# Optimization experiments

Hardware: AMD Instinct MI355X
Metric: run time of the kernel (lower is better)

## Reference

```python
import jax, jax.numpy as jnp
import numpy as np

EPS = 1e-6
NEG = -1e9
RES_RATIO = 1.0  # res_ratio init arg
MAKE_SYM = True


def _ln(x, g, b):
    m = jnp.mean(x, axis=-1, keepdims=True)
    v = jnp.mean((x - m) ** 2, axis=-1, keepdims=True)
    return (x - m) * jax.lax.rsqrt(v + EPS) * g + b


def _sim(q, k, W1q, W1k, b1, W2, b2):
    # NN(concat([q,k])) with first dense split into query/key halves:
    # relu(q@W1q + k@W1k + b1) @ W2 + b2  -> avoids materializing the 2d concat.
    qa = q @ W1q  # [b,n,sq,h]
    kb = k @ W1k  # [b,n,sk,h]
    h1 = jax.nn.relu(qa[:, :, :, None, :] + kb[:, :, None, :, :] + b1)  # [b,n,sq,sk,h]
    s = jnp.einsum('bnqkh,h->bnqk', h1, W2[:, 0]) + b2[0]
    if MAKE_SYM:
        qb = q @ W1k
        ka = k @ W1q
        h2 = jax.nn.relu(ka[:, :, None, :, :] + qb[:, :, :, None, :] + b1)
        s = s + jnp.einsum('bnqkh,h->bnqk', h2, W2[:, 0]) + b2[0]
    return s


def _attention(v, k, q, mask, Ww, bw, Wd, bd, W1q, W1k, b1, W2, b2):
    q = q @ Ww + bw
    k = k @ Ww + bw
    v = v @ Ww + bw
    logits = _sim(q, k, W1q, W1k, b1, W2, b2)
    if mask is not None:
        logits = logits + mask * NEG
    attn = jax.nn.softmax(logits, axis=-1)
    out = jnp.einsum('bnqk,bnkd->bnqd', attn, v)
    return out @ Wd + bd, attn


def setup_inputs() -> dict:
    key = jax.random.key(0)
    B, N, S, D, DFF, H = 4, 1, 256, 128, 512, 128
    ks = jax.random.split(key, 16)
    s = 0.02
    inp = {
        'x': jax.random.normal(ks[0], (B, N, S, D), jnp.float32),
        'enc_output': jax.random.normal(ks[1], (B, N, S, D), jnp.float32),
        'com_mask': jnp.zeros((B, N, S, S), jnp.float32),
        'dec_mask': jnp.zeros((B, N, S, S), jnp.float32),
        # shared pairwise-score MLP NN: Dense(H, relu) -> Dense(1)
        'W1q': jax.random.normal(ks[2], (D, H), jnp.float32) * s,
        'W1k': jax.random.normal(ks[3], (D, H), jnp.float32) * s,
        'b1': jnp.zeros((H,), jnp.float32),
        'W2': jax.random.normal(ks[4], (H, 1), jnp.float32) * s,
        'b2': jnp.zeros((1,), jnp.float32),
        # mha1 projections
        'Ww1': jax.random.normal(ks[5], (D, D), jnp.float32) * s,
        'bw1': jnp.zeros((D,), jnp.float32),
        'Wd1': jax.random.normal(ks[6], (D, D), jnp.float32) * s,
        'bd1': jnp.zeros((D,), jnp.float32),
        # mha2 projections
        'Ww2': jax.random.normal(ks[7], (D, D), jnp.float32) * s,
        'bw2': jnp.zeros((D,), jnp.float32),
        'Wd2': jax.random.normal(ks[8], (D, D), jnp.float32) * s,
        'bd2': jnp.zeros((D,), jnp.float32),
        # ffn
        'Wf1': jax.random.normal(ks[9], (D, DFF), jnp.float32) * s,
        'bf1': jnp.zeros((DFF,), jnp.float32),
        'Wf2': jax.random.normal(ks[10], (DFF, D), jnp.float32) * s,
        'bf2': jnp.zeros((D,), jnp.float32),
        # layernorms
        'ln1_g': jnp.ones((D,), jnp.float32), 'ln1_b': jnp.zeros((D,), jnp.float32),
        'ln2_g': jnp.ones((D,), jnp.float32), 'ln2_b': jnp.zeros((D,), jnp.float32),
        'ln3_g': jnp.ones((D,), jnp.float32), 'ln3_b': jnp.zeros((D,), jnp.float32),
    }
    return inp


def reference(x, enc_output, com_mask, dec_mask,
              W1q, W1k, b1, W2, b2,
              Ww1, bw1, Wd1, bd1,
              Ww2, bw2, Wd2, bd2,
              Wf1, bf1, Wf2, bf2,
              ln1_g, ln1_b, ln2_g, ln2_b, ln3_g, ln3_b):
    r = RES_RATIO
    # self-attention block (dropout inactive, eval mode)
    attn1, aw1 = _attention(x, x, x, com_mask, Ww1, bw1, Wd1, bd1, W1q, W1k, b1, W2, b2)
    out1 = _ln((2 - r) * attn1 + r * x, ln1_g, ln1_b)
    # cross-attention block
    attn2, aw2 = _attention(enc_output, enc_output, out1, dec_mask, Ww2, bw2, Wd2, bd2, W1q, W1k, b1, W2, b2)
    out2 = _ln((2 - r) * attn2 + r * out1, ln2_g, ln2_b)
    # ffn
    ffn = jax.nn.relu(out2 @ Wf1 + bf1) @ Wf2 + bf2
    out3 = _ln((2 - r) * ffn + r * out2, ln3_g, ln3_b)
    return out3
```

## Files before the change

### kernel.cpp

```cpp
#include <hip/hip_runtime.h>
#include <math.h>


#define LN_EPS 1e-6f
#define NEGV  (-1e9f)

constexpr int B = 4, S = 256, D = 128, H = 128, DFF = 512;
constexpr int R = B * S;

struct P {
    const float *x, *enc, *com_mask, *dec_mask;
    const float *W1q, *W1k, *b1, *W2;
    const float *Ww1, *bw1, *Wd1, *bd1;
    const float *Ww2, *bw2, *Wd2, *bd2;
    const float *Wf1, *bf1, *Wf2, *bf2;
    const float *ln1g, *ln1b, *ln2g, *ln2b, *ln3g, *ln3b;
    float *out;
    float *xw, *qa, *kb, *kv2w, *kb2, *ka2;
};

__global__ __launch_bounds__(512) void proj3_kernel(P p)
{
    const int g = blockIdx.y, tid = threadIdx.x;
    const int r0 = blockIdx.x * 8;
    __shared__ __align__(16) float Ash[8 * 128];
    __shared__ __align__(16) float Pw[8 * 128];
    __shared__ __align__(16) float Pp[2 * 8 * 128];

    const float* A    = g ? p.enc  : p.x;
    const float* Wp   = g ? p.Ww2  : p.Ww1;
    const float* bp   = g ? p.bw2  : p.bw1;
    float*       o_w  = g ? p.kv2w : p.xw;
    const float* Wsec = g ? p.W1k  : p.W1q;
    const float* bsec = g ? nullptr: p.b1;
    float*       o_s  = g ? p.kb2  : p.qa;
    const float* Wthr = g ? p.W1q  : p.W1k;
    float*       o_t  = g ? p.ka2  : p.kb;

    if (tid < 256)
        ((float4*)Ash)[tid] = ((const float4*)(A + (size_t)r0 * 128))[tid];
    __syncthreads();

    {
        const int kh = tid >> 8, unit = tid & 255, lr = unit >> 5, c4 = unit & 31;
        const float4* W4 = (const float4*)Wp;
        float4 acc = (kh == 0) ? ((const float4*)bp)[c4] : make_float4(0.f, 0.f, 0.f, 0.f);
        const int k0 = kh * 64;
        #pragma unroll 8
        for (int k = 0; k < 64; ++k) {
            const float a = Ash[lr * 128 + k0 + k];
            const float4 w = W4[(k0 + k) * 32 + c4];
            acc.x = fmaf(a, w.x, acc.x); acc.y = fmaf(a, w.y, acc.y);
            acc.z = fmaf(a, w.z, acc.z); acc.w = fmaf(a, w.w, acc.w);
        }
        ((float4*)Pp)[kh * 256 + unit] = acc;
    }
    __syncthreads();
    if (tid < 256) {
        const int lr = tid >> 5, c4 = tid & 31;
        const float4 a = ((const float4*)Pp)[tid];
        const float4 bq = ((const float4*)Pp)[256 + tid];
        const float4 w = make_float4(a.x + bq.x, a.y + bq.y, a.z + bq.z, a.w + bq.w);
        ((float4*)Pw)[tid] = w;
        ((float4*)o_w)[(size_t)(r0 + lr) * 32 + c4] = w;
    }
    __syncthreads();

    {
        const int which = tid >> 8, unit = tid & 255, lr = unit >> 5, c4 = unit & 31;
        const float* W = which ? Wthr : Wsec;
        const float* bb = which ? nullptr : bsec;
        float* o = which ? o_t : o_s;
        const float4* W4 = (const float4*)W;
        float4 acc = bb ? ((const float4*)bb)[c4] : make_float4(0.f, 0.f, 0.f, 0.f);
        #pragma unroll 8
        for (int k = 0; k < 128; ++k) {
            const float a = Pw[lr * 128 + k];
            const float4 w = W4[k * 32 + c4];
            acc.x = fmaf(a, w.x, acc.x); acc.y = fmaf(a, w.y, acc.y);
            acc.z = fmaf(a, w.z, acc.z); acc.w = fmaf(a, w.w, acc.w);
        }
        ((float4*)o)[(size_t)(r0 + lr) * 32 + c4] = acc;
    }
}

#define SC8(ACC, O1, X1, O2, X2)                                               \
    ACC = fmaf(fmaxf((O1).x + (X1).x, 0.f), w.x, ACC);                         \
    ACC = fmaf(fmaxf((O1).y + (X1).y, 0.f), w.y, ACC);                         \
    ACC = fmaf(fmaxf((O1).z + (X1).z, 0.f), w.z, ACC);                         \
    ACC = fmaf(fmaxf((O1).w + (X1).w, 0.f), w.w, ACC);                         \
    ACC = fmaf(fmaxf((O2).x + (X2).x, 0.f), w.x, ACC);                         \
    ACC = fmaf(fmaxf((O2).y + (X2).y, 0.f), w.y, ACC);                         \
    ACC = fmaf(fmaxf((O2).z + (X2).z, 0.f), w.z, ACC);                         \
    ACC = fmaf(fmaxf((O2).w + (X2).w, 0.f), w.w, ACC);

template<bool FIRST>
__device__ __forceinline__ void attn_stage(const P& p, float* smem,
                                           int tid, int r0, int bS)
{
    float* s8   = smem;
    float* rowS = smem + 1024;
    float* qa2L = smem + 18432;
    float* qb2L = smem + 18944;

    const float* __restrict__ S1g = FIRST ? p.kb : p.kb2;
    const float* __restrict__ S2g = FIRST ? p.qa : p.ka2;
    const float* mask = FIRST ? p.com_mask : p.dec_mask;
    const float* V    = FIRST ? p.xw : p.kv2w;
    const float* Wd   = FIRST ? p.Wd1 : p.Wd2;
    const float* bd   = FIRST ? p.bd1 : p.bd2;
    const float* lg   = FIRST ? p.ln1g : p.ln2g;
    const float* lb   = FIRST ? p.ln1b : p.ln2b;

    {
        const int hh = tid & 7, unit = tid >> 3, kk = unit & 31, rg = unit >> 5;
        const int rA = r0 + 2 * rg, rB = rA + 1;

        float4 o1A[4], o1B[4], o2A[4], o2B[4], w2r[4];
        #pragma unroll
        for (int j = 0; j < 4; ++j) {
            const int h = hh * 4 + 32 * j;
            if (FIRST) {
                o1A[j] = *(const float4*)(p.qa + (size_t)rA * H + h);
                o1B[j] = *(const float4*)(p.qa + (size_t)rB * H + h);
                o2A[j] = *(const float4*)(p.kb + (size_t)rA * H + h);
                o2B[j] = *(const float4*)(p.kb + (size_t)rB * H + h);
            } else {
                o1A[j] = *(const float4*)(qa2L + (2 * rg)     * H + h);
                o1B[j] = *(const float4*)(qa2L + (2 * rg + 1) * H + h);
                o2A[j] = *(const float4*)(qb2L + (2 * rg)     * H + h);
                o2B[j] = *(const float4*)(qb2L + (2 * rg + 1) * H + h);
            }
            w2r[j] = *(const float4*)(p.W2 + h);
        }

        for (int kt = 0; kt < 4; ++kt) {
            const float* __restrict__ r1a = S1g + (size_t)(bS + kt * 64 + kk)      * H;
            const float* __restrict__ r1b = S1g + (size_t)(bS + kt * 64 + kk + 32) * H;
            const float* __restrict__ r2a = S2g + (size_t)(bS + kt * 64 + kk)      * H;
            const float* __restrict__ r2b = S2g + (size_t)(bS + kt * 64 + kk + 32) * H;

            float4 x1a[4], x1b[4], x2a[4], x2b[4];
            #pragma unroll
            for (int j = 0; j < 4; ++j) {
                const int h = hh * 4 + 32 * j;
                x1a[j] = *(const float4*)(r1a + h);
                x1b[j] = *(const float4*)(r1b + h);
                x2a[j] = *(const float4*)(r2a + h);
                x2b[j] = *(const float4*)(r2b + h);
            }

            float aAa = 0.f, aAb = 0.f, aBa = 0.f, aBb = 0.f;
            #pragma unroll
            for (int j = 0; j < 4; ++j) {
                const float4 w = w2r[j];
                SC8(aAa, o1A[j], x1a[j], o2A[j], x2a[j])
                SC8(aAb, o1A[j], x1b[j], o2A[j], x2b[j])
                SC8(aBa, o1B[j], x1a[j], o2B[j], x2a[j])
                SC8(aBb, o1B[j], x1b[j], o2B[j], x2b[j])
            }
            #pragma unroll
            for (int o = 1; o < 8; o <<= 1) {
                aAa += __shfl_xor(aAa, o, 8);
                aAb += __shfl_xor(aAb, o, 8);
                aBa += __shfl_xor(aBa, o, 8);
                aBb += __shfl_xor(aBb, o, 8);
            }
            if (hh == 0) {
                const int kb0 = kt * 64;
                s8[(2 * rg)     * 256 + kb0 + kk]      = aAa;
                s8[(2 * rg)     * 256 + kb0 + kk + 32] = aAb;
                s8[(2 * rg + 1) * 256 + kb0 + kk]      = aBa;
                s8[(2 * rg + 1) * 256 + kb0 + kk + 32] = aBb;
            }
        }
    }
    __syncthreads();

    for (int i = tid; i < 1024; i += 512) {
        const int r = i >> 8, k = i & 255;
        s8[i] += mask[(size_t)(r0 + r) * S + k] * NEGV;
    }
    __syncthreads();

    {
        const int g = tid >> 6, c = tid & 63;
        if (g < 4) {
            float* rowp = s8 + g * 256;
            float m = -INFINITY;
            #pragma unroll
            for (int k = c; k < 256; k += 64) m = fmaxf(m, rowp[k]);
            for (int o = 32; o; o >>= 1) m = fmaxf(m, __shfl_xor(m, o, 64));
            float s = 0.f;
            #pragma unroll
            for (int k = c; k < 256; k += 64) { const float e = __expf(rowp[k] - m); rowp[k] = e; s += e; }
            for (int o = 32; o; o >>= 1) s += __shfl_xor(s, o, 64);
            const float rinv = 1.f / s;
            #pragma unroll
            for (int k = c; k < 256; k += 64) rowp[k] *= rinv;
        }
    }
    __syncthreads();

    float* avp = smem + 1536;
    float* aoS = smem + 3584;
    float* pp  = smem + 4096;

    {
        const int r = tid >> 7, t = tid & 127, kq = t >> 5, c4 = t & 31;
        const float4* V4 = (const float4*)(V + (size_t)bS * D);
        const float* sp = s8 + r * 256 + kq * 64;
        float4 acc = make_float4(0.f, 0.f, 0.f, 0.f);
        #pragma unroll 8
        for (int k = 0; k < 64; ++k) {
            const float a = sp[k];
            const float4 v = V4[(kq * 64 + k) * 32 + c4];
            acc.x = fmaf(a, v.x, acc.x); acc.y = fmaf(a, v.y, acc.y);
            acc.z = fmaf(a, v.z, acc.z); acc.w = fmaf(a, v.w, acc.w);
        }
        ((float4*)avp)[(r * 4 + kq) * 32 + c4] = acc;
    }
    __syncthreads();
    if (tid < 128) {
        const int r = tid >> 5, c4 = tid & 31;
        float4 s0 = ((const float4*)avp)[(r * 4 + 0) * 32 + c4];
        const float4 s1 = ((const float4*)avp)[(r * 4 + 1) * 32 + c4];
        const float4 s2 = ((const float4*)avp)[(r * 4 + 2) * 32 + c4];
        const float4 s3 = ((const float4*)avp)[(r * 4 + 3) * 32 + c4];
        s0.x += s1.x + s2.x + s3.x; s0.y += s1.y + s2.y + s3.y;
        s0.z += s1.z + s2.z + s3.z; s0.w += s1.w + s2.w + s3.w;
        ((float4*)aoS)[r * 32 + c4] = s0;
    }
    __syncthreads();

    {
        const int kq = tid >> 7, unit = tid & 127, r = unit >> 5, c4 = unit & 31;
        const float4* W4 = (const float4*)Wd;
        const float* ap = aoS + r * 128 + kq * 32;
        float4 acc = make_float4(0.f, 0.f, 0.f, 0.f);
        #pragma unroll 8
        for (int k = 0; k < 32; ++k) {
            const float a = ap[k];
            const float4 w = W4[(kq * 32 + k) * 32 + c4];
            acc.x = fmaf(a, w.x, acc.x); acc.y = fmaf(a, w.y, acc.y);
            acc.z = fmaf(a, w.z, acc.z); acc.w = fmaf(a, w.w, acc.w);
        }
        ((float4*)pp)[kq * 128 + unit] = acc;
    }
    __syncthreads();

    if (tid < 128) {
        const int r = tid >> 5, c4 = tid & 31;
        const float4 p0 = ((const float4*)pp)[tid];
        const float4 p1 = ((const float4*)pp)[128 + tid];
        const float4 p2 = ((const float4*)pp)[256 + tid];
        const float4 p3 = ((const float4*)pp)[384 + tid];
        const float4 bv0 = ((const float4*)bd)[c4];
        float4 r4;
        if (FIRST) r4 = ((const float4*)(p.x + (size_t)(r0 + r) * 128))[c4];
        else       r4 = ((const float4*)rowS)[r * 32 + c4];
        const float x0 = p0.x + p1.x + p2.x + p3.x + bv0.x + r4.x;
        const float x1 = p0.y + p1.y + p2.y + p3.y + bv0.y + r4.y;
        const float x2 = p0.z + p1.z + p2.z + p3.z + bv0.z + r4.z;
        const float x3 = p0.w + p1.w + p2.w + p3.w + bv0.w + r4.w;
        float s  = x0 + x1 + x2 + x3;
        float s2 = x0 * x0 + x1 * x1 + x2 * x2 + x3 * x3;
        for (int o = 16; o; o >>= 1) { s += __shfl_xor(s, o, 32); s2 += __shfl_xor(s2, o, 32); }
        const float m = s * (1.f / 128), var = s2 * (1.f / 128) - m * m;
        const float rs = rsqrtf(var + LN_EPS);
        const float4 gv = ((const float4*)lg)[c4], bv = ((const float4*)lb)[c4];
        float4 o4;
        o4.x = (x0 - m) * rs * gv.x + bv.x; o4.y = (x1 - m) * rs * gv.y + bv.y;
        o4.z = (x2 - m) * rs * gv.z + bv.z; o4.w = (x3 - m) * rs * gv.w + bv.w;
        ((float4*)rowS)[r * 32 + c4] = o4;
    }
    __syncthreads();

    if (FIRST) {
        float* qpp  = smem + 6144;
        float* q2wS = smem + 8192;
        float* qp2  = smem + 8704;
        {
            const int kq = tid >> 7, unit = tid & 127, r = unit >> 5, c4 = unit & 31;
            const float4* W4 = (const float4*)p.Ww2;
            const float* ap = rowS + r * 128 + kq * 32;
            float4 acc = make_float4(0.f, 0.f, 0.f, 0.f);
            #pragma unroll 8
            for (int k = 0; k < 32; ++k) {
                const float a = ap[k];
                const float4 w = W4[(kq * 32 + k) * 32 + c4];
                acc.x = fmaf(a, w.x, acc.x); acc.y = fmaf(a, w.y, acc.y);
                acc.z = fmaf(a, w.z, acc.z); acc.w = fmaf(a, w.w, acc.w);
            }
            ((float4*)qpp)[kq * 128 + unit] = acc;
        }
        __syncthreads();
        if (tid < 128) {
            const int c4 = tid & 31;
            const float4 p0 = ((const float4*)qpp)[tid];
            const float4 p1 = ((const float4*)qpp)[128 + tid];
            const float4 p2 = ((const float4*)qpp)[256 + tid];
            const float4 p3 = ((const float4*)qpp)[384 + tid];
            const float4 bw = ((const float4*)p.bw2)[c4];
            ((float4*)q2wS)[tid] = make_float4(p0.x + p1.x + p2.x + p3.x + bw.x,
                                               p0.y + p1.y + p2.y + p3.y + bw.y,
                                               p0.z + p1.z + p2.z + p3.z + bw.z,
                                               p0.w + p1.w + p2.w + p3.w + bw.w);
        }
        __syncthreads();
        {
            const int which = tid >> 8, sub = tid & 255;
            const int kh = sub >> 7, unit2 = sub & 127;
            const float4* W4 = (const float4*)(which ? p.W1k : p.W1q);
            const int r = unit2 >> 5;
            const float* ap = q2wS + r * 128 + kh * 64;
            float4 acc = make_float4(0.f, 0.f, 0.f, 0.f);
            #pragma unroll 8
            for (int k = 0; k < 64; ++k) {
                const float a = ap[k];
                const float4 w = W4[(kh * 64 + k) * 32 + (unit2 & 31)];
                acc.x = fmaf(a, w.x, acc.x); acc.y = fmaf(a, w.y, acc.y);
                acc.z = fmaf(a, w.z, acc.z); acc.w = fmaf(a, w.w, acc.w);
            }
            ((float4*)qp2)[(which * 2 + kh) * 128 + unit2] = acc;
        }
        __syncthreads();
        if (tid < 256) {
            const int which = tid >> 7, unit2 = tid & 127;
            const int c4 = unit2 & 31;
            const float4 p0 = ((const float4*)qp2)[(which * 2 + 0) * 128 + unit2];
            const float4 p1 = ((const float4*)qp2)[(which * 2 + 1) * 128 + unit2];
            const float4 b1v = ((const float4*)p.b1)[c4];
            float* oq = which ? qb2L : qa2L;
            ((float4*)oq)[unit2] =
                make_float4(p0.x + p1.x + b1v.x, p0.y + p1.y + b1v.y,
                            p0.z + p1.z + b1v.z, p0.w + p1.w + b1v.w);
        }
        __syncthreads();
    } else {
        float* hidP = smem + 1536;
        float* part = smem + 9984;
        {
            const int c = tid & 127, kh = tid >> 7;
            const float4* Wf1_4 = (const float4*)p.Wf1;
            float4 a0 = make_float4(0.f,0.f,0.f,0.f), a1 = a0, a2 = a0, a3 = a0;
            const int kbase = kh * 32;
            #pragma unroll 8
            for (int k = 0; k < 32; ++k) {
                const int kk = kbase + k;
                const float4 w = Wf1_4[kk * 128 + c];
                const float s0 = rowS[kk],       s1 = rowS[128 + kk];
                const float s2 = rowS[256 + kk], s3 = rowS[384 + kk];
                a0.x=fmaf(s0,w.x,a0.x); a0.y=fmaf(s0,w.y,a0.y); a0.z=fmaf(s0,w.z,a0.z); a0.w=fmaf(s0,w.w,a0.w);
                a1.x=fmaf(s1,w.x,a1.x); a1.y=fmaf(s1,w.y,a1.y); a1.z=fmaf(s1,w.z,a1.z); a1.w=fmaf(s1,w.w,a1.w);
                a2.x=fmaf(s2,w.x,a2.x); a2.y=fmaf(s2,w.y,a2.y); a2.z=fmaf(s2,w.z,a2.z); a2.w=fmaf(s2,w.w,a2.w);
                a3.x=fmaf(s3,w.x,a3.x); a3.y=fmaf(s3,w.y,a3.y); a3.z=fmaf(s3,w.z,a3.z); a3.w=fmaf(s3,w.w,a3.w);
            }
            float4* h4 = (float4*)hidP;
            const int base = kh * 512;
            h4[base + 0*128 + c] = a0; h4[base + 1*128 + c] = a1;
            h4[base + 2*128 + c] = a2; h4[base + 3*128 + c] = a3;
        }
        __syncthreads();
        for (int i = tid; i < 2048; i += 512) {
            hidP[i] = fmaxf(hidP[i] + hidP[2048 + i] + hidP[4096 + i] + hidP[6144 + i]
                            + p.bf1[i & 511], 0.f);
        }
        __syncthreads();
        {
            const int c4f = tid & 31, kg = tid >> 5;
            const float4* Wf2_4 = (const float4*)p.Wf2;
            float4 a0 = make_float4(0.f,0.f,0.f,0.f), a1 = a0, a2 = a0, a3 = a0;
            const int kbase = kg * 32;
            const float* h0 = hidP + 0 * 512 + kbase;
            const float* h1 = hidP + 1 * 512 + kbase;
            const float* h2 = hidP + 2 * 512 + kbase;
            const float* h3 = hidP + 3 * 512 + kbase;
            #pragma unroll 8
            for (int k = 0; k < 32; ++k) {
                const float4 w = Wf2_4[(kbase + k) * 32 + c4f];
                const float s0 = h0[k], s1 = h1[k], s2 = h2[k], s3 = h3[k];
                a0.x=fmaf(s0,w.x,a0.x); a0.y=fmaf(s0,w.y,a0.y); a0.z=fmaf(s0,w.z,a0.z); a0.w=fmaf(s0,w.w,a0.w);
                a1.x=fmaf(s1,w.x,a1.x); a1.y=fmaf(s1,w.y,a1.y); a1.z=fmaf(s1,w.z,a1.z); a1.w=fmaf(s1,w.w,a1.w);
                a2.x=fmaf(s2,w.x,a2.x); a2.y=fmaf(s2,w.y,a2.y); a2.z=fmaf(s2,w.z,a2.z); a2.w=fmaf(s2,w.w,a2.w);
                a3.x=fmaf(s3,w.x,a3.x); a3.y=fmaf(s3,w.y,a3.y); a3.z=fmaf(s3,w.z,a3.z); a3.w=fmaf(s3,w.w,a3.w);
            }
            float4* p4 = (float4*)part;
            p4[kg * 128 + 0 * 32 + c4f] = a0; p4[kg * 128 + 1 * 32 + c4f] = a1;
            p4[kg * 128 + 2 * 32 + c4f] = a2; p4[kg * 128 + 3 * 32 + c4f] = a3;
        }
        __syncthreads();
        if (tid < 128) {
            const int r = tid >> 5, c4 = tid & 31;
            const float4* p4 = (const float4*)part;
            float4 sum = ((const float4*)p.bf2)[c4];
            #pragma unroll
            for (int kg = 0; kg < 16; ++kg) {
                const float4 v = p4[kg * 128 + r * 32 + c4];
                sum.x += v.x; sum.y += v.y; sum.z += v.z; sum.w += v.w;
            }
            const float4 r4 = ((const float4*)rowS)[r * 32 + c4];
            const float x0 = sum.x + r4.x, x1 = sum.y + r4.y;
            const float x2 = sum.z + r4.z, x3 = sum.w + r4.w;
            float s  = x0 + x1 + x2 + x3;
            float s2 = x0 * x0 + x1 * x1 + x2 * x2 + x3 * x3;
            for (int o = 16; o; o >>= 1) { s += __shfl_xor(s, o, 32); s2 += __shfl_xor(s2, o, 32); }
            const float m = s * (1.f / 128), var = s2 * (1.f / 128) - m * m;
            const float rs = rsqrtf(var + LN_EPS);
            const float4 gv = ((const float4*)p.ln3g)[c4], bv = ((const float4*)p.ln3b)[c4];
            float4 o4;
            o4.x = (x0 - m) * rs * gv.x + bv.x; o4.y = (x1 - m) * rs * gv.y + bv.y;
            o4.z = (x2 - m) * rs * gv.z + bv.z; o4.w = (x3 - m) * rs * gv.w + bv.w;
            ((float4*)p.out)[(size_t)(r0 + r) * 32 + c4] = o4;
        }
    }
}

__global__ __launch_bounds__(512) void fused_attn12_kernel(P p)
{
    __shared__ __align__(16) float smem[19456];
    const int tid = threadIdx.x;
    const int r0 = blockIdx.x * 4, bS = (r0 >> 8) * S;
    attn_stage<true >(p, smem, tid, r0, bS);
    attn_stage<false>(p, smem, tid, r0, bS);
}

extern "C" void kernel_launch(void* const* d_in, const int* in_sizes, int n_in,
                              void* d_out, int out_size, void* d_ws, size_t ws_size,
                              hipStream_t stream) {
    (void)in_sizes; (void)n_in; (void)out_size; (void)ws_size;
    P p;
    p.x        = (const float*)d_in[0];
    p.enc      = (const float*)d_in[1];
    p.com_mask = (const float*)d_in[2];
    p.dec_mask = (const float*)d_in[3];
    p.W1q = (const float*)d_in[4];
    p.W1k = (const float*)d_in[5];
    p.b1  = (const float*)d_in[6];
    p.W2  = (const float*)d_in[7];
    p.Ww1 = (const float*)d_in[9];
    p.bw1 = (const float*)d_in[10];
    p.Wd1 = (const float*)d_in[11];
    p.bd1 = (const float*)d_in[12];
    p.Ww2 = (const float*)d_in[13];
    p.bw2 = (const float*)d_in[14];
    p.Wd2 = (const float*)d_in[15];
    p.bd2 = (const float*)d_in[16];
    p.Wf1 = (const float*)d_in[17];
    p.bf1 = (const float*)d_in[18];
    p.Wf2 = (const float*)d_in[19];
    p.bf2 = (const float*)d_in[20];
    p.ln1g = (const float*)d_in[21];
    p.ln1b = (const float*)d_in[22];
    p.ln2g = (const float*)d_in[23];
    p.ln2b = (const float*)d_in[24];
    p.ln3g = (const float*)d_in[25];
    p.ln3b = (const float*)d_in[26];
    p.out  = (float*)d_out;

    float* ws = (float*)d_ws;
    const size_t RD = (size_t)R * D;
    p.xw    = ws;
    p.qa    = p.xw    + RD;
    p.kb    = p.qa    + RD;
    p.kv2w  = p.kb    + RD;
    p.kb2   = p.kv2w  + RD;
    p.ka2   = p.kb2   + RD;

    proj3_kernel<<<dim3(R / 8, 2), 512, 0, stream>>>(p);
    fused_attn12_kernel<<<R / 4, 512, 0, stream>>>(p);
}
```

Measured before the change: 164.5 us.

## Halve rows per block in projection and fused attention kernels to double grid size

Both kernels now handle half as many rows per block (4 in the projection kernel, 2 in the attention kernel), so twice as many blocks are launched. Thread work is re-split into more K-slices with wider shared-memory partial reductions. The mask add is folded into the score write, softmax normalisation is deferred to a per-row reciprocal applied after attn·V, and the shared-memory footprint is shrunk. The aim is more blocks and better occupancy across the CUs, at the cost of reloading K/V and weights from global memory more often per row.

Measured after the change: 178.1 us. +8.2%, slower.

```diff
diff --git a/kernel.cpp b/kernel.cpp
--- a/kernel.cpp
+++ b/kernel.cpp
@@ -22,10 +22,11 @@
 __global__ __launch_bounds__(512) void proj3_kernel(P p)
 {
     const int g = blockIdx.y, tid = threadIdx.x;
-    const int r0 = blockIdx.x * 8;
-    __shared__ __align__(16) float Ash[8 * 128];
-    __shared__ __align__(16) float Pw[8 * 128];
-    __shared__ __align__(16) float Pp[2 * 8 * 128];
+    const int r0 = blockIdx.x * 4;
+    __shared__ __align__(16) float Ash[4 * 128];
+    __shared__ __align__(16) float Pw[4 * 128];
+    __shared__ __align__(16) float Pp[4 * 4 * 128];
+    __shared__ __align__(16) float P2[2 * 2 * 4 * 128];
 
     const float* A    = g ? p.enc  : p.x;
     const float* Wp   = g ? p.Ww2  : p.Ww1;
@@ -37,50 +38,67 @@
     const float* Wthr = g ? p.W1q  : p.W1k;
     float*       o_t  = g ? p.ka2  : p.kb;
 
-    if (tid < 256)
+    if (tid < 128)
         ((float4*)Ash)[tid] = ((const float4*)(A + (size_t)r0 * 128))[tid];
     __syncthreads();
 
     {
-        const int kh = tid >> 8, unit = tid & 255, lr = unit >> 5, c4 = unit & 31;
+        const int kh = tid >> 7, unit = tid & 127, lr = unit >> 5, c4 = unit & 31;
         const float4* W4 = (const float4*)Wp;
         float4 acc = (kh == 0) ? ((const float4*)bp)[c4] : make_float4(0.f, 0.f, 0.f, 0.f);
-        const int k0 = kh * 64;
+        const int k0 = kh * 32;
         #pragma unroll 8
-        for (int k = 0; k < 64; ++k) {
+        for (int k = 0; k < 32; ++k) {
             const float a = Ash[lr * 128 + k0 + k];
             const float4 w = W4[(k0 + k) * 32 + c4];
             acc.x = fmaf(a, w.x, acc.x); acc.y = fmaf(a, w.y, acc.y);
             acc.z = fmaf(a, w.z, acc.z); acc.w = fmaf(a, w.w, acc.w);
         }
-        ((float4*)Pp)[kh * 256 + unit] = acc;
-    }
-    __syncthreads();
-    if (tid < 256) {
+        ((float4*)Pp)[kh * 128 + unit] = acc;
+    }
+    __syncthreads();
+    if (tid < 128) {
         const int lr = tid >> 5, c4 = tid & 31;
-        const float4 a = ((const float4*)Pp)[tid];
-        const float4 bq = ((const float4*)Pp)[256 + tid];
-        const float4 w = make_float4(a.x + bq.x, a.y + bq.y, a.z + bq.z, a.w + bq.w);
+        const float4 a0 = ((const float4*)Pp)[tid];
+        const float4 a1 = ((const float4*)Pp)[128 + tid];
+        const float4 a2 = ((const float4*)Pp)[256 + tid];
+        const float4 a3 = ((const float4*)Pp)[384 + tid];
+        const float4 w = make_float4(a0.x + a1.x + a2.x + a3.x,
+                                     a0.y + a1.y + a2.y + a3.y,
+                                     a0.z + a1.z + a2.z + a3.z,
+                                     a0.w + a1.w + a2.w + a3.w);
         ((float4*)Pw)[tid] = w;
         ((float4*)o_w)[(size_t)(r0 + lr) * 32 + c4] = w;
     }
     __syncthreads();
 
     {
-        const int which = tid >> 8, unit = tid & 255, lr = unit >> 5, c4 = unit & 31;
+        const int which = tid >> 8, sub = tid & 255;
+        const int kh = sub >> 7, unit2 = sub & 127, lr = unit2 >> 5, c4 = unit2 & 31;
         const float* W = which ? Wthr : Wsec;
         const float* bb = which ? nullptr : bsec;
-        float* o = which ? o_t : o_s;
         const float4* W4 = (const float4*)W;
-        float4 acc = bb ? ((const float4*)bb)[c4] : make_float4(0.f, 0.f, 0.f, 0.f);
+        float4 acc = (kh == 0 && bb) ? ((const float4*)bb)[c4]
+                                     : make_float4(0.f, 0.f, 0.f, 0.f);
+        const int k0 = kh * 64;
         #pragma unroll 8
-        for (int k = 0; k < 128; ++k) {
-            const float a = Pw[lr * 128 + k];
-            const float4 w = W4[k * 32 + c4];
+        for (int k = 0; k < 64; ++k) {
+            const float a = Pw[lr * 128 + k0 + k];
+            const float4 w = W4[(k0 + k) * 32 + c4];
             acc.x = fmaf(a, w.x, acc.x); acc.y = fmaf(a, w.y, acc.y);
             acc.z = fmaf(a, w.z, acc.z); acc.w = fmaf(a, w.w, acc.w);
         }
-        ((float4*)o)[(size_t)(r0 + lr) * 32 + c4] = acc;
+        ((float4*)P2)[(which * 2 + kh) * 128 + unit2] = acc;
+    }
+    __syncthreads();
+    if (tid < 256) {
+        const int which = tid >> 7, unit2 = tid & 127;
+        const int lr = unit2 >> 5, c4 = unit2 & 31;
+        const float4 p0 = ((const float4*)P2)[(which * 2 + 0) * 128 + unit2];
+        const float4 p1 = ((const float4*)P2)[(which * 2 + 1) * 128 + unit2];
+        float* o = which ? o_t : o_s;
+        ((float4*)o)[(size_t)(r0 + lr) * 32 + c4] =
+            make_float4(p0.x + p1.x, p0.y + p1.y, p0.z + p1.z, p0.w + p1.w);
     }
 }
 
@@ -98,10 +116,12 @@
 __device__ __forceinline__ void attn_stage(const P& p, float* smem,
                                            int tid, int r0, int bS)
 {
-    float* s8   = smem;
-    float* rowS = smem + 1024;
-    float* qa2L = smem + 18432;
-    float* qb2L = smem + 18944;
+    float* s8    = smem;
+    float* rowS  = smem + 512;
+    float* rinvS = smem + 768;
+    float* qa2L  = smem + 784;
+    float* qb2L  = smem + 1040;
+    constexpr int SB = 1296;
 
     const float* __restrict__ S1g = FIRST ? p.kb : p.kb2;
     const float* __restrict__ S2g = FIRST ? p.qa : p.ka2;
@@ -113,8 +133,8 @@
     const float* lb   = FIRST ? p.ln1b : p.ln2b;
 
     {
-        const int hh = tid & 7, unit = tid >> 3, kk = unit & 31, rg = unit >> 5;
-        const int rA = r0 + 2 * rg, rB = rA + 1;
+        const int hh = tid & 7, kk = tid >> 3;
+        const int rA = r0, rB = r0 + 1;
 
         float4 o1A[4], o1B[4], o2A[4], o2B[4], w2r[4];
         #pragma unroll
@@ -126,66 +146,51 @@
                 o2A[j] = *(const float4*)(p.kb + (size_t)rA * H + h);
                 o2B[j] = *(const float4*)(p.kb + (size_t)rB * H + h);
             } else {
-                o1A[j] = *(const float4*)(qa2L + (2 * rg)     * H + h);
-                o1B[j] = *(const float4*)(qa2L + (2 * rg + 1) * H + h);
-                o2A[j] = *(const float4*)(qb2L + (2 * rg)     * H + h);
-                o2B[j] = *(const float4*)(qb2L + (2 * rg + 1) * H + h);
+                o1A[j] = *(const float4*)(qa2L + h);
+                o1B[j] = *(const float4*)(qa2L + 128 + h);
+                o2A[j] = *(const float4*)(qb2L + h);
+                o2B[j] = *(const float4*)(qb2L + 128 + h);
             }
             w2r[j] = *(const float4*)(p.W2 + h);
         }
 
+        #pragma unroll
         for (int kt = 0; kt < 4; ++kt) {
-            const float* __restrict__ r1a = S1g + (size_t)(bS + kt * 64 + kk)      * H;
-            const float* __restrict__ r1b = S1g + (size_t)(bS + kt * 64 + kk + 32) * H;
-            const float* __restrict__ r2a = S2g + (size_t)(bS + kt * 64 + kk)      * H;
-            const float* __restrict__ r2b = S2g + (size_t)(bS + kt * 64 + kk + 32) * H;
-
-            float4 x1a[4], x1b[4], x2a[4], x2b[4];
+            const float* __restrict__ r1 = S1g + (size_t)(bS + kt * 64 + kk) * H;
+            const float* __restrict__ r2 = S2g + (size_t)(bS + kt * 64 + kk) * H;
+
+            float4 x1[4], x2[4];
             #pragma unroll
             for (int j = 0; j < 4; ++j) {
                 const int h = hh * 4 + 32 * j;
-                x1a[j] = *(const float4*)(r1a + h);
-                x1b[j] = *(const float4*)(r1b + h);
-                x2a[j] = *(const float4*)(r2a + h);
-                x2b[j] = *(const float4*)(r2b + h);
-            }
-
-            float aAa = 0.f, aAb = 0.f, aBa = 0.f, aBb = 0.f;
+                x1[j] = *(const float4*)(r1 + h);
+                x2[j] = *(const float4*)(r2 + h);
+            }
+
+            float aA = 0.f, aB = 0.f;
             #pragma unroll
             for (int j = 0; j < 4; ++j) {
                 const float4 w = w2r[j];
-                SC8(aAa, o1A[j], x1a[j], o2A[j], x2a[j])
-                SC8(aAb, o1A[j], x1b[j], o2A[j], x2b[j])
-                SC8(aBa, o1B[j], x1a[j], o2B[j], x2a[j])
-                SC8(aBb, o1B[j], x1b[j], o2B[j], x2b[j])
+                SC8(aA, o1A[j], x1[j], o2A[j], x2[j])
+                SC8(aB, o1B[j], x1[j], o2B[j], x2[j])
             }
             #pragma unroll
             for (int o = 1; o < 8; o <<= 1) {
-                aAa += __shfl_xor(aAa, o, 8);
-                aAb += __shfl_xor(aAb, o, 8);
-                aBa += __shfl_xor(aBa, o, 8);
-                aBb += __shfl_xor(aBb, o, 8);
+                aA += __shfl_xor(aA, o, 8);
+                aB += __shfl_xor(aB, o, 8);
             }
             if (hh == 0) {
-                const int kb0 = kt * 64;
-                s8[(2 * rg)     * 256 + kb0 + kk]      = aAa;
-                s8[(2 * rg)     * 256 + kb0 + kk + 32] = aAb;
-                s8[(2 * rg + 1) * 256 + kb0 + kk]      = aBa;
-                s8[(2 * rg + 1) * 256 + kb0 + kk + 32] = aBb;
-            }
-        }
-    }
-    __syncthreads();
-
-    for (int i = tid; i < 1024; i += 512) {
-        const int r = i >> 8, k = i & 255;
-        s8[i] += mask[(size_t)(r0 + r) * S + k] * NEGV;
+                const int k = kt * 64 + kk;
+                s8[k]       = aA + mask[(size_t)rA * S + k] * NEGV;
+                s8[256 + k] = aB + mask[(size_t)rB * S + k] * NEGV;
+            }
+        }
     }
     __syncthreads();
 
     {
         const int g = tid >> 6, c = tid & 63;
-        if (g < 4) {
+        if (g < 2) {
             float* rowp = s8 + g * 256;
             float m = -INFINITY;
             #pragma unroll
@@ -195,74 +200,72 @@
             #pragma unroll
             for (int k = c; k < 256; k += 64) { const float e = __expf(rowp[k] - m); rowp[k] = e; s += e; }
             for (int o = 32; o; o >>= 1) s += __shfl_xor(s, o, 64);
-            const float rinv = 1.f / s;
-            #pragma unroll
-            for (int k = c; k < 256; k += 64) rowp[k] *= rinv;
-        }
-    }
-    __syncthreads();
-
-    float* avp = smem + 1536;
-    float* aoS = smem + 3584;
-    float* pp  = smem + 4096;
-
-    {
-        const int r = tid >> 7, t = tid & 127, kq = t >> 5, c4 = t & 31;
+            if (c == 0) rinvS[g] = 1.f / s;
+        }
+    }
+    __syncthreads();
+
+    float* avp = smem + SB;
+    float* aoS = smem + SB + 2048;
+    float* pp  = smem + SB + 2304;
+
+    {
+        const int r = tid >> 8, t = tid & 255, kq = t >> 5, c4 = t & 31;
         const float4* V4 = (const float4*)(V + (size_t)bS * D);
-        const float* sp = s8 + r * 256 + kq * 64;
-        float4 acc = make_float4(0.f, 0.f, 0.f, 0.f);
-        #pragma unroll 8
-        for (int k = 0; k < 64; ++k) {
-            const float a = sp[k];
-            const float4 v = V4[(kq * 64 + k) * 32 + c4];
-            acc.x = fmaf(a, v.x, acc.x); acc.y = fmaf(a, v.y, acc.y);
-            acc.z = fmaf(a, v.z, acc.z); acc.w = fmaf(a, v.w, acc.w);
-        }
-        ((float4*)avp)[(r * 4 + kq) * 32 + c4] = acc;
-    }
-    __syncthreads();
-    if (tid < 128) {
-        const int r = tid >> 5, c4 = tid & 31;
-        float4 s0 = ((const float4*)avp)[(r * 4 + 0) * 32 + c4];
-        const float4 s1 = ((const float4*)avp)[(r * 4 + 1) * 32 + c4];
-        const float4 s2 = ((const float4*)avp)[(r * 4 + 2) * 32 + c4];
-        const float4 s3 = ((const float4*)avp)[(r * 4 + 3) * 32 + c4];
-        s0.x += s1.x + s2.x + s3.x; s0.y += s1.y + s2.y + s3.y;
-        s0.z += s1.z + s2.z + s3.z; s0.w += s1.w + s2.w + s3.w;
-        ((float4*)aoS)[r * 32 + c4] = s0;
-    }
-    __syncthreads();
-
-    {
-        const int kq = tid >> 7, unit = tid & 127, r = unit >> 5, c4 = unit & 31;
-        const float4* W4 = (const float4*)Wd;
-        const float* ap = aoS + r * 128 + kq * 32;
+        const float* sp = s8 + r * 256 + kq * 32;
         float4 acc = make_float4(0.f, 0.f, 0.f, 0.f);
         #pragma unroll 8
         for (int k = 0; k < 32; ++k) {
+            const float a = sp[k];
+            const float4 v = V4[(kq * 32 + k) * 32 + c4];
+            acc.x = fmaf(a, v.x, acc.x); acc.y = fmaf(a, v.y, acc.y);
+            acc.z = fmaf(a, v.z, acc.z); acc.w = fmaf(a, v.w, acc.w);
+        }
+        ((float4*)avp)[(r * 8 + kq) * 32 + c4] = acc;
+    }
+    __syncthreads();
+    if (tid < 64) {
+        const int r = tid >> 5, c4 = tid & 31;
+        float4 s0 = make_float4(0.f, 0.f, 0.f, 0.f);
+        #pragma unroll
+        for (int i = 0; i < 8; ++i) {
+            const float4 v = ((const float4*)avp)[(r * 8 + i) * 32 + c4];
+            s0.x += v.x; s0.y += v.y; s0.z += v.z; s0.w += v.w;
+        }
+        const float rv = rinvS[r];
+        ((float4*)aoS)[r * 32 + c4] = make_float4(s0.x * rv, s0.y * rv, s0.z * rv, s0.w * rv);
+    }
+    __syncthreads();
+
+    {
+        const int kq = tid >> 6, unit = tid & 63, r = unit >> 5, c4 = unit & 31;
+        const float4* W4 = (const float4*)Wd;
+        const float* ap = aoS + r * 128 + kq * 16;
+        float4 acc = make_float4(0.f, 0.f, 0.f, 0.f);
+        #pragma unroll 8
+        for (int k = 0; k < 16; ++k) {
             const float a = ap[k];
-            const float4 w = W4[(kq * 32 + k) * 32 + c4];
+            const float4 w = W4[(kq * 16 + k) * 32 + c4];
             acc.x = fmaf(a, w.x, acc.x); acc.y = fmaf(a, w.y, acc.y);
             acc.z = fmaf(a, w.z, acc.z); acc.w = fmaf(a, w.w, acc.w);
         }
-        ((float4*)pp)[kq * 128 + unit] = acc;
-    }
-    __syncthreads();
-
-    if (tid < 128) {
+        ((float4*)pp)[kq * 64 + unit] = acc;
+    }
+    __syncthreads();
+
+    if (tid < 64) {
         const int r = tid >> 5, c4 = tid & 31;
-        const float4 p0 = ((const float4*)pp)[tid];
-        const float4 p1 = ((const float4*)pp)[128 + tid];
-        const float4 p2 = ((const float4*)pp)[256 + tid];
-        const float4 p3 = ((const float4*)pp)[384 + tid];
-        const float4 bv0 = ((const float4*)bd)[c4];
+        float4 sum = ((const float4*)bd)[c4];
+        #pragma unroll
+        for (int i = 0; i < 8; ++i) {
+            const float4 v = ((const float4*)pp)[i * 64 + tid];
+            sum.x += v.x; sum.y += v.y; sum.z += v.z; sum.w += v.w;
+        }
         float4 r4;
         if (FIRST) r4 = ((const float4*)(p.x + (size_t)(r0 + r) * 128))[c4];
         else       r4 = ((const float4*)rowS)[r * 32 + c4];
-        const float x0 = p0.x + p1.x + p2.x + p3.x + bv0.x + r4.x;
-        const float x1 = p0.y + p1.y + p2.y + p3.y + bv0.y + r4.y;
-        const float x2 = p0.z + p1.z + p2.z + p3.z + bv0.z + r4.z;
-        const float x3 = p0.w + p1.w + p2.w + p3.w + bv0.w + r4.w;
+        const float x0 = sum.x + r4.x, x1 = sum.y + r4.y;
+        const float x2 = sum.z + r4.z, x3 = sum.w + r4.w;
         float s  = x0 + x1 + x2 + x3;
         float s2 = x0 * x0 + x1 * x1 + x2 * x2 + x3 * x3;
         for (int o = 16; o; o >>= 1) { s += __shfl_xor(s, o, 32); s2 += __shfl_xor(s2, o, 32); }
@@ -277,126 +280,114 @@
     __syncthreads();
 
     if (FIRST) {
-        float* qpp  = smem + 6144;
-        float* q2wS = smem + 8192;
-        float* qp2  = smem + 8704;
+        float* qpp  = smem + SB;
+        float* q2wS = smem + SB + 2048;
+        float* qp2  = smem + SB + 2304;
         {
-            const int kq = tid >> 7, unit = tid & 127, r = unit >> 5, c4 = unit & 31;
+            const int kq = tid >> 6, unit = tid & 63, r = unit >> 5, c4 = unit & 31;
             const float4* W4 = (const float4*)p.Ww2;
-            const float* ap = rowS + r * 128 + kq * 32;
+            const float* ap = rowS + r * 128 + kq * 16;
+            float4 acc = make_float4(0.f, 0.f, 0.f, 0.f);
+            #pragma unroll 8
+            for (int k = 0; k < 16; ++k) {
+                const float a = ap[k];
+                const float4 w = W4[(kq * 16 + k) * 32 + c4];
+                acc.x = fmaf(a, w.x, acc.x); acc.y = fmaf(a, w.y, acc.y);
+                acc.z = fmaf(a, w.z, acc.z); acc.w = fmaf(a, w.w, acc.w);
+            }
+            ((float4*)qpp)[kq * 64 + unit] = acc;
+        }
+        __syncthreads();
+        if (tid < 64) {
+            const int c4 = tid & 31;
+            float4 sum = ((const float4*)p.bw2)[c4];
+            #pragma unroll
+            for (int i = 0; i < 8; ++i) {
+                const float4 v = ((const float4*)qpp)[i * 64 + tid];
+                sum.x += v.x; sum.y += v.y; sum.z += v.z; sum.w += v.w;
+            }
+            ((float4*)q2wS)[tid] = sum;
+        }
+        __syncthreads();
+        {
+            const int which = tid >> 8, sub = tid & 255;
+            const int kh = sub >> 6, unit2 = sub & 63, r = unit2 >> 5, c4 = unit2 & 31;
+            const float4* W4 = (const float4*)(which ? p.W1k : p.W1q);
+            const float* ap = q2wS + r * 128 + kh * 32;
             float4 acc = make_float4(0.f, 0.f, 0.f, 0.f);
             #pragma unroll 8
             for (int k = 0; k < 32; ++k) {
                 const float a = ap[k];
-                const float4 w = W4[(kq * 32 + k) * 32 + c4];
+                const float4 w = W4[(kh * 32 + k) * 32 + c4];
                 acc.x = fmaf(a, w.x, acc.x); acc.y = fmaf(a, w.y, acc.y);
                 acc.z = fmaf(a, w.z, acc.z); acc.w = fmaf(a, w.w, acc.w);
             }
-            ((float4*)qpp)[kq * 128 + unit] = acc;
+            ((float4*)qp2)[(which * 4 + kh) * 64 + unit2] = acc;
         }
         __syncthreads();
         if (tid < 128) {
-            const int c4 = tid & 31;
-            const float4 p0 = ((const float4*)qpp)[tid];
-            const float4 p1 = ((const float4*)qpp)[128 + tid];
-            const float4 p2 = ((const float4*)qpp)[256 + tid];
-            const float4 p3 = ((const float4*)qpp)[384 + tid];
-            const float4 bw = ((const float4*)p.bw2)[c4];
-            ((float4*)q2wS)[tid] = make_float4(p0.x + p1.x + p2.x + p3.x + bw.x,
-                                               p0.y + p1.y + p2.y + p3.y + bw.y,
-                                               p0.z + p1.z + p2.z + p3.z + bw.z,
-                                               p0.w + p1.w + p2.w + p3.w + bw.w);
-        }
-        __syncthreads();
-        {
-            const int which = tid >> 8, sub = tid & 255;
-            const int kh = sub >> 7, unit2 = sub & 127;
-            const float4* W4 = (const float4*)(which ? p.W1k : p.W1q);
-            const int r = unit2 >> 5;
-            const float* ap = q2wS + r * 128 + kh * 64;
-            float4 acc = make_float4(0.f, 0.f, 0.f, 0.f);
-            #pragma unroll 8
-            for (int k = 0; k < 64; ++k) {
-                const float a = ap[k];
-                const float4 w = W4[(kh * 64 + k) * 32 + (unit2 & 31)];
-                acc.x = fmaf(a, w.x, acc.x); acc.y = fmaf(a, w.y, acc.y);
-                acc.z = fmaf(a, w.z, acc.z); acc.w = fmaf(a, w.w, acc.w);
-            }
-            ((float4*)qp2)[(which * 2 + kh) * 128 + unit2] = acc;
-        }
-        __syncthreads();
-        if (tid < 256) {
-            const int which = tid >> 7, unit2 = tid & 127;
-            const int c4 = unit2 & 31;
-            const float4 p0 = ((const float4*)qp2)[(which * 2 + 0) * 128 + unit2];
-            const float4 p1 = ((const float4*)qp2)[(which * 2 + 1) * 128 + unit2];
-            const float4 b1v = ((const float4*)p.b1)[c4];
+            const int which = tid >> 6, unit2 = tid & 63, c4 = unit2 & 31;
+            float4 sum = ((const float4*)p.b1)[c4];
+            #pragma unroll
+            for (int i = 0; i < 4; ++i) {
+                const float4 v = ((const float4*)qp2)[(which * 4 + i) * 64 + unit2];
+                sum.x += v.x; sum.y += v.y; sum.z += v.z; sum.w += v.w;
+            }
             float* oq = which ? qb2L : qa2L;
-            ((float4*)oq)[unit2] =
-                make_float4(p0.x + p1.x + b1v.x, p0.y + p1.y + b1v.y,
-                            p0.z + p1.z + b1v.z, p0.w + p1.w + b1v.w);
+            ((float4*)oq)[unit2] = sum;
         }
         __syncthreads();
     } else {
-        float* hidP = smem + 1536;
-        float* part = smem + 9984;
+        float* hidP = smem + SB;
+        float* part = smem + SB + 4096;
         {
             const int c = tid & 127, kh = tid >> 7;
             const float4* Wf1_4 = (const float4*)p.Wf1;
-            float4 a0 = make_float4(0.f,0.f,0.f,0.f), a1 = a0, a2 = a0, a3 = a0;
+            float4 a0 = make_float4(0.f,0.f,0.f,0.f), a1 = a0;
             const int kbase = kh * 32;
             #pragma unroll 8
             for (int k = 0; k < 32; ++k) {
                 const int kk = kbase + k;
                 const float4 w = Wf1_4[kk * 128 + c];
-                const float s0 = rowS[kk],       s1 = rowS[128 + kk];
-                const float s2 = rowS[256 + kk], s3 = rowS[384 + kk];
+                const float s0 = rowS[kk], s1 = rowS[128 + kk];
                 a0.x=fmaf(s0,w.x,a0.x); a0.y=fmaf(s0,w.y,a0.y); a0.z=fmaf(s0,w.z,a0.z); a0.w=fmaf(s0,w.w,a0.w);
                 a1.x=fmaf(s1,w.x,a1.x); a1.y=fmaf(s1,w.y,a1.y); a1.z=fmaf(s1,w.z,a1.z); a1.w=fmaf(s1,w.w,a1.w);
-                a2.x=fmaf(s2,w.x,a2.x); a2.y=fmaf(s2,w.y,a2.y); a2.z=fmaf(s2,w.z,a2.z); a2.w=fmaf(s2,w.w,a2.w);
-                a3.x=fmaf(s3,w.x,a3.x); a3.y=fmaf(s3,w.y,a3.y); a3.z=fmaf(s3,w.z,a3.z); a3.w=fmaf(s3,w.w,a3.w);
             }
             float4* h4 = (float4*)hidP;
-            const int base = kh * 512;
-            h4[base + 0*128 + c] = a0; h4[base + 1*128 + c] = a1;
-            h4[base + 2*128 + c] = a2; h4[base + 3*128 + c] = a3;
-        }
-        __syncthreads();
-        for (int i = tid; i < 2048; i += 512) {
-            hidP[i] = fmaxf(hidP[i] + hidP[2048 + i] + hidP[4096 + i] + hidP[6144 + i]
+            h4[kh * 256 + c]       = a0;
+            h4[kh * 256 + 128 + c] = a1;
+        }
+        __syncthreads();
+        for (int i = tid; i < 1024; i += 512) {
+            hidP[i] = fmaxf(hidP[i] + hidP[1024 + i] + hidP[2048 + i] + hidP[3072 + i]
                             + p.bf1[i & 511], 0.f);
         }
         __syncthreads();
         {
             const int c4f = tid & 31, kg = tid >> 5;
             const float4* Wf2_4 = (const float4*)p.Wf2;
-            float4 a0 = make_float4(0.f,0.f,0.f,0.f), a1 = a0, a2 = a0, a3 = a0;
+            float4 a0 = make_float4(0.f,0.f,0.f,0.f), a1 = a0;
             const int kbase = kg * 32;
-            const float* h0 = hidP + 0 * 512 + kbase;
-            const float* h1 = hidP + 1 * 512 + kbase;
-            const float* h2 = hidP + 2 * 512 + kbase;
-            const float* h3 = hidP + 3 * 512 + kbase;
+            const float* h0 = hidP + kbase;
+            const float* h1 = hidP + 512 + kbase;
             #pragma unroll 8
             for (int k = 0; k < 32; ++k) {
                 const float4 w = Wf2_4[(kbase + k) * 32 + c4f];
-                const float s0 = h0[k], s1 = h1[k], s2 = h2[k], s3 = h3[k];
+                const float s0 = h0[k], s1 = h1[k];
                 a0.x=fmaf(s0,w.x,a0.x); a0.y=fmaf(s0,w.y,a0.y); a0.z=fmaf(s0,w.z,a0.z); a0.w=fmaf(s0,w.w,a0.w);
                 a1.x=fmaf(s1,w.x,a1.x); a1.y=fmaf(s1,w.y,a1.y); a1.z=fmaf(s1,w.z,a1.z); a1.w=fmaf(s1,w.w,a1.w);
-                a2.x=fmaf(s2,w.x,a2.x); a2.y=fmaf(s2,w.y,a2.y); a2.z=fmaf(s2,w.z,a2.z); a2.w=fmaf(s2,w.w,a2.w);
-                a3.x=fmaf(s3,w.x,a3.x); a3.y=fmaf(s3,w.y,a3.y); a3.z=fmaf(s3,w.z,a3.z); a3.w=fmaf(s3,w.w,a3.w);
             }
             float4* p4 = (float4*)part;
-            p4[kg * 128 + 0 * 32 + c4f] = a0; p4[kg * 128 + 1 * 32 + c4f] = a1;
-            p4[kg * 128 + 2 * 32 + c4f] = a2; p4[kg * 128 + 3 * 32 + c4f] = a3;
-        }
-        __syncthreads();
-        if (tid < 128) {
+            p4[kg * 64 + c4f]      = a0;
+            p4[kg * 64 + 32 + c4f] = a1;
+        }
+        __syncthreads();
+        if (tid < 64) {
             const int r = tid >> 5, c4 = tid & 31;
-            const float4* p4 = (const float4*)part;
             float4 sum = ((const float4*)p.bf2)[c4];
             #pragma unroll
             for (int kg = 0; kg < 16; ++kg) {
-                const float4 v = p4[kg * 128 + r * 32 + c4];
+                const float4 v = ((const float4*)part)[kg * 64 + r * 32 + c4];
                 sum.x += v.x; sum.y += v.y; sum.z += v.z; sum.w += v.w;
             }
             const float4 r4 = ((const float4*)rowS)[r * 32 + c4];
@@ -418,9 +409,9 @@
 
 __global__ __launch_bounds__(512) void fused_attn12_kernel(P p)
 {
-    __shared__ __align__(16) float smem[19456];
+    __shared__ __align__(16) float smem[9488];
     const int tid = threadIdx.x;
-    const int r0 = blockIdx.x * 4, bS = (r0 >> 8) * S;
+    const int r0 = blockIdx.x * 2, bS = (r0 >> 8) * S;
     attn_stage<true >(p, smem, tid, r0, bS);
     attn_stage<false>(p, smem, tid, r0, bS);
 }
@@ -467,6 +458,6 @@
     p.kb2   = p.kv2w  + RD;
     p.ka2   = p.kb2   + RD;
 
-    proj3_kernel<<<dim3(R / 8, 2), 512, 0, stream>>>(p);
-    fused_attn12_kernel<<<R / 4, 512, 0, stream>>>(p);
+    proj3_kernel<<<dim3(R / 4, 2), 512, 0, stream>>>(p);
+    fused_attn12_kernel<<<R / 2, 512, 0, stream>>>(p);
 }
```
